# Kernel tuning notes

Measured on AMD Instinct MI355X. Metric: run time of the kernel, lower is better.

## Reference

```python
import jax, jax.numpy as jnp
import numpy as np

T, H_IN = 2048, 84
HID = 256
NA = 18


def _conv(x, w, b, stride):
    # x: [N,C,H,W], w: [O,I,kh,kw]
    y = jax.lax.conv_general_dilated(
        x, w, window_strides=(stride, stride), padding='VALID',
        dimension_numbers=('NCHW', 'OIHW', 'NCHW'))
    return jax.nn.relu(y + b[None, :, None, None])


def setup_inputs() -> dict:
    key = jax.random.key(0)
    ks = jax.random.split(key, 17)
    p = lambda k, shape, s=0.05: (jax.random.normal(k, shape, jnp.float32) * s)
    return {
        'input_frames': jax.random.uniform(ks[0], (T, 1, H_IN, H_IN), jnp.float32),
        'conv1_w': p(ks[1], (32, 1, 8, 8)),   'conv1_b': p(ks[2], (32,)),
        'conv2_w': p(ks[3], (64, 32, 4, 4)),  'conv2_b': p(ks[4], (64,)),
        'conv3_w': p(ks[5], (256, 64, 3, 3)), 'conv3_b': p(ks[6], (256,)),
        'attn_w1': p(ks[7], (HID, HID)),      'attn_b1': p(ks[8], (HID,)),
        'attn_w2': p(ks[9], (HID, HID)),      'attn_b2': p(ks[10], (HID,)),
        'lstm_w_ih': p(ks[11], (4 * HID, HID)), 'lstm_w_hh': p(ks[12], (4 * HID, HID)),
        'lstm_b_ih': p(ks[13], (4 * HID,)),     'lstm_b_hh': p(ks[14], (4 * HID,)),
        'q_w': p(ks[15], (NA, HID)),          'q_b': p(ks[16], (NA,)),
    }


def reference(input_frames, conv1_w, conv1_b, conv2_w, conv2_b, conv3_w, conv3_b,
              attn_w1, attn_b1, attn_w2, attn_b2,
              lstm_w_ih, lstm_w_hh, lstm_b_ih, lstm_b_hh, q_w, q_b):
    # CNN over all frames at once (loop in torch was over frames; math identical)
    x = _conv(input_frames, conv1_w, conv1_b, 4)   # [T,32,20,20]
    x = _conv(x, conv2_w, conv2_b, 2)              # [T,64,9,9]
    fm = _conv(x, conv3_w, conv3_b, 1)             # [T,256,7,7]
    t, c, hh, ww = fm.shape
    # build_vector: vectors[i, ch] = fm[ch, y, x], i = y*W + x
    vecs = fm.reshape(t, c, hh * ww).transpose(0, 2, 1)  # [T,49,256]

    def step(carry, v):
        h, cc = carry  # [256], [256]
        # additive attention; softmax over the 256 feature dim per spatial vector
        s = jnp.tanh(v @ attn_w1.T + attn_b1 + h)              # [49,256]
        w = jax.nn.softmax(s @ attn_w2.T + attn_b2, axis=-1)   # [49,256]
        ctx = jnp.sum(w * v, axis=0)                           # [256]
        # single-layer LSTM cell, torch gate order i,f,g,o
        gates = ctx @ lstm_w_ih.T + lstm_b_ih + h @ lstm_w_hh.T + lstm_b_hh
        i, f, g, o = jnp.split(gates, 4)
        c_new = jax.nn.sigmoid(f) * cc + jax.nn.sigmoid(i) * jnp.tanh(g)
        h_new = jax.nn.sigmoid(o) * jnp.tanh(c_new)
        return (h_new, c_new), None

    h0 = jnp.zeros((HID,), fm.dtype)
    (h_T, _), _ = jax.lax.scan(step, (h0, h0), vecs)
    q = h_T @ q_w.T + q_b          # [18]
    return q[None, :]              # [1, nr_actions], matches torch output
```

## Files before the change

kernel.cpp:

```cpp
#include <hip/hip_runtime.h>
#include <hip/hip_bf16.h>
#include <math.h>


#define T_FRAMES 2048
#define NI 49
#define HID 256
#define NA 18
#define NWG 8

typedef __bf16 v8bf __attribute__((ext_vector_type(8)));
typedef float v4f __attribute__((ext_vector_type(4)));

static constexpr size_t OFF_FM1   = 0;
static constexpr size_t OFF_FM2   = 104857600;
static constexpr size_t OFF_VECS  = 147324928;
static constexpr size_t OFF_W2B   = 250085376;
static constexpr size_t OFF_WIHB  = OFF_W2B  + 131072;
static constexpr size_t OFF_WHHB  = OFF_WIHB + 524288;
static constexpr size_t OFF_W1T   = OFF_WHHB + 524288;
static constexpr size_t OFF_HBUF  = OFF_FM2;
static constexpr size_t OFF_CPUB  = OFF_FM2 + 1024;
static constexpr size_t OFF_FLH   = OFF_FM2 + 9216;
static constexpr size_t OFF_FLC   = OFF_FM2 + 10240;

__global__ void prep_weights(const float* __restrict__ w2, const float* __restrict__ wih,
                             const float* __restrict__ whh, const float* __restrict__ w1,
                             __bf16* w2b, __bf16* wihb, __bf16* whhb, float* w1t) {
  int idx = blockIdx.x * 256 + threadIdx.x;
  int stride = gridDim.x * 256;
  for (int i = idx; i < 65536; i += stride) w2b[i] = (__bf16)w2[i];
  for (int i = idx; i < 262144; i += stride) wihb[i] = (__bf16)wih[i];
  for (int i = idx; i < 262144; i += stride) whhb[i] = (__bf16)whh[i];
  for (int i = idx; i < 65536; i += stride) {
    int r = i >> 8, c = i & 255;
    w1t[c * 256 + r] = w1[i];
  }
}

__global__ void conv1_k(const float* __restrict__ x, const float* __restrict__ w,
                        const float* __restrict__ b, float* __restrict__ y) {
  int idx = blockIdx.x * 256 + threadIdx.x;
  if (idx >= T_FRAMES * 32 * 20 * 20) return;
  int xx = idx % 20, yy = (idx / 20) % 20, o = (idx / 400) % 32, t = idx / 12800;
  const float* xp = x + t * 7056 + yy * 4 * 84 + xx * 4;
  const float* wp = w + o * 64;
  float acc = b[o];
  #pragma unroll
  for (int ky = 0; ky < 8; ky++)
    #pragma unroll
    for (int kx = 0; kx < 8; kx++)
      acc += xp[ky * 84 + kx] * wp[ky * 8 + kx];
  y[idx] = fmaxf(acc, 0.f);
}

__global__ __launch_bounds__(256) void conv2_k(const float* __restrict__ fm1, const float* __restrict__ w,
                                               const float* __restrict__ b, float* __restrict__ fm2) {
  __shared__ float xs[32 * 400];
  int t = blockIdx.x, tid = threadIdx.x;
  for (int i = tid; i < 12800; i += 256) xs[i] = fm1[t * 12800 + i];
  __syncthreads();
  int o = tid >> 2, q = tid & 3;
  int p0 = q * 21, p1 = (p0 + 21 < 81) ? p0 + 21 : 81;
  int ob[21];
  #pragma unroll
  for (int i2 = 0; i2 < 21; i2++) {
    int p = p0 + i2; if (p > 80) p = 80;
    int yy = p / 9, xx2 = p - yy * 9;
    ob[i2] = yy * 40 + xx2 * 2;
  }
  float acc[21];
  #pragma unroll
  for (int i2 = 0; i2 < 21; i2++) acc[i2] = 0.f;
  for (int c = 0; c < 32; c++) {
    int cbase = c * 400;
    for (int ky = 0; ky < 4; ky++)
      for (int kx = 0; kx < 4; kx++) {
        float wgt = w[((o * 32 + c) * 4 + ky) * 4 + kx];
        int kyo = ky * 20 + kx;
        #pragma unroll
        for (int i2 = 0; i2 < 21; i2++)
          acc[i2] += wgt * xs[cbase + ob[i2] + kyo];
      }
  }
  float bo = b[o];
  #pragma unroll
  for (int i2 = 0; i2 < 21; i2++) {
    int p = p0 + i2;
    if (p < p1) fm2[t * 5184 + o * 81 + p] = fmaxf(acc[i2] + bo, 0.f);
  }
}

__global__ __launch_bounds__(256) void conv3_k(const float* __restrict__ fm2, const float* __restrict__ w,
                                               const float* __restrict__ b, float* __restrict__ vecs) {
  __shared__ float xs[64 * 81];
  __shared__ float ws4[256][37];
  int t = blockIdx.x, tid = threadIdx.x;
  for (int i = tid; i < 64 * 81; i += 256) xs[i] = fm2[t * 5184 + i];
  float acc[49];
  #pragma unroll
  for (int i = 0; i < 49; i++) acc[i] = 0.f;
  for (int c0 = 0; c0 < 64; c0 += 4) {
    __syncthreads();
    for (int i = tid; i < 256 * 36; i += 256) {
      int oo = i / 36, j = i - oo * 36;
      ws4[oo][j] = w[oo * 576 + c0 * 9 + j];
    }
    __syncthreads();
    for (int cc = 0; cc < 4; cc++)
      for (int ky = 0; ky < 3; ky++)
        for (int kx = 0; kx < 3; kx++) {
          float wgt = ws4[tid][cc * 9 + ky * 3 + kx];
          const float* xp = &xs[(c0 + cc) * 81 + ky * 9 + kx];
          #pragma unroll
          for (int yy = 0; yy < 7; yy++)
            #pragma unroll
            for (int xx = 0; xx < 7; xx++)
              acc[yy * 7 + xx] += wgt * xp[yy * 9 + xx];
        }
  }
  float bo = b[tid];
  for (int i = 0; i < 49; i++)
    vecs[(t * 49 + i) * 256 + tid] = fmaxf(acc[i] + bo, 0.f);
}

__global__ __launch_bounds__(256) void aprep_k(const float* __restrict__ vecs, const float* __restrict__ w1t,
                                               const float* __restrict__ b1, float* __restrict__ A) {
  __shared__ float vs[49][256];
  int t = blockIdx.x, tid = threadIdx.x;
  for (int i = tid; i < 49 * 256; i += 256) vs[i >> 8][i & 255] = vecs[t * 12544 + i];
  __syncthreads();
  float acc[49];
  #pragma unroll
  for (int i = 0; i < 49; i++) acc[i] = 0.f;
  for (int k = 0; k < 256; k++) {
    float wgt = w1t[k * 256 + tid];
    #pragma unroll
    for (int i = 0; i < 49; i++) acc[i] += vs[i][k] * wgt;
  }
  float bb = b1[tid];
  for (int i = 0; i < 49; i++) A[(t * 49 + i) * 256 + tid] = acc[i] + bb;
}

__global__ void init_comm(unsigned* flh, unsigned* flc) {
  int idx = blockIdx.x * 512 + threadIdx.x;
  if (idx < NWG * 32) { flh[idx] = 0u; flc[idx] = 0u; }
}

__device__ __forceinline__ float tanh_fast(float x) {
  float e = __expf(2.f * x);
  return 1.f - 2.f / (e + 1.f);
}

__global__ __launch_bounds__(256, 1) void scan_k(
    const float* __restrict__ A, const float* __restrict__ vecs,
    const __bf16* __restrict__ w2b, const __bf16* __restrict__ wihb, const __bf16* __restrict__ whhb,
    const float* __restrict__ b2g, const float* __restrict__ bihg, const float* __restrict__ bhhg,
    const float* __restrict__ qw, const float* __restrict__ qb,
    float* hbuf, unsigned* cpub, unsigned* flh, unsigned* flc, float* out) {
  __shared__ __bf16 Ss[16][264];
  __shared__ float hs[HID];
  __shared__ __bf16 hbf[HID];
  __shared__ float Wt[8][HID];
  __shared__ float cxp[8][HID];
  __shared__ float b2s[HID];
  __shared__ float gb[4][32];

  const int w = blockIdx.x;
  const int tid = threadIdx.x;
  const int lane = tid & 63;
  const int wv = tid >> 6;
  const int quad = lane >> 4;
  const int l15 = lane & 15;
  const int r0 = 6 * w;
  const int nr = (w < 7) ? 6 : 7;
  const int prow = tid >> 5;
  const int pcol = (tid & 31) * 8;

  for (int i = tid; i < 16 * 264; i += 256) (&Ss[0][0])[i] = (__bf16)0.f;
  for (int i = tid; i < 8 * HID; i += 256) (&cxp[0][0])[i] = 0.f;
  b2s[tid] = b2g[tid];
  hs[tid] = 0.f;
  hbf[tid] = (__bf16)0.f;
  float cbias[4];
  if (tid < 32) {
    #pragma unroll
    for (int g = 0; g < 4; g++) {
      int row = 256 * g + 32 * w + tid;
      cbias[g] = bihg[row] + bhhg[row];
    }
  }
  float creg = 0.f;

  v8bf BW2[4][8];
  #pragma unroll
  for (int ntl = 0; ntl < 4; ntl++) {
    const int row = wv * 64 + ntl * 16 + l15;
    #pragma unroll
    for (int k = 0; k < 8; k++)
      BW2[ntl][k] = *(const v8bf*)(w2b + row * 256 + k * 32 + quad * 8);
  }
  v8bf BIH[2][8], BHH[2][8];
  #pragma unroll
  for (int nt = 0; nt < 2; nt++) {
    const int row = 256 * wv + 32 * w + nt * 16 + l15;
    #pragma unroll
    for (int k = 0; k < 8; k++) {
      BIH[nt][k] = *(const v8bf*)(wihb + row * 256 + k * 32 + quad * 8);
      BHH[nt][k] = *(const v8bf*)(whhb + row * 256 + k * 32 + quad * 8);
    }
  }
  __syncthreads();

  for (int t = 0; t < T_FRAMES; t++) {
    int rr = r0 + prow; if (rr > 48) rr = 48;
    const float* Ap = A + ((long)t * NI + rr) * HID + pcol;
    const float* Vp = vecs + ((long)t * NI + rr) * HID + pcol;
    const float4 a40 = *(const float4*)(Ap);
    const float4 a41 = *(const float4*)(Ap + 4);
    const float4 v40 = *(const float4*)(Vp);
    const float4 v41 = *(const float4*)(Vp + 4);

    if (t > 0) {
      if (wv == 0) {
        const unsigned tgt = (unsigned)t;
        int guard = 0;
        while (true) {
          unsigned fv = (lane < NWG)
              ? __hip_atomic_load(&flh[lane * 32], __ATOMIC_RELAXED, __HIP_MEMORY_SCOPE_AGENT)
              : tgt;
          if (__all(fv >= tgt) || ++guard > 5000000) break;
          __builtin_amdgcn_s_sleep(1);
        }
      }
      __syncthreads();
      float hv = __hip_atomic_load(&hbuf[tid], __ATOMIC_RELAXED, __HIP_MEMORY_SCOPE_AGENT);
      hs[tid] = hv;
      hbf[tid] = (__bf16)hv;
      __syncthreads();
    }

    if (prow < nr) {
      const float* hp = &hs[pcol];
      v8bf sv;
      sv[0] = (__bf16)tanh_fast(a40.x + hp[0]);
      sv[1] = (__bf16)tanh_fast(a40.y + hp[1]);
      sv[2] = (__bf16)tanh_fast(a40.z + hp[2]);
      sv[3] = (__bf16)tanh_fast(a40.w + hp[3]);
      sv[4] = (__bf16)tanh_fast(a41.x + hp[4]);
      sv[5] = (__bf16)tanh_fast(a41.y + hp[5]);
      sv[6] = (__bf16)tanh_fast(a41.z + hp[6]);
      sv[7] = (__bf16)tanh_fast(a41.w + hp[7]);
      *(v8bf*)&Ss[prow][pcol] = sv;
    }
    __syncthreads();

    v4f acc[4];
    #pragma unroll
    for (int ntl = 0; ntl < 4; ntl++) acc[ntl] = (v4f){0.f, 0.f, 0.f, 0.f};
    #pragma unroll
    for (int k = 0; k < 8; k++) {
      const v8bf av = *(const v8bf*)&Ss[l15][k * 32 + quad * 8];
      #pragma unroll
      for (int ntl = 0; ntl < 4; ntl++)
        acc[ntl] = __builtin_amdgcn_mfma_f32_16x16x32_bf16(av, BW2[ntl][k], acc[ntl], 0, 0, 0);
    }
    if (quad < 2) {
      #pragma unroll
      for (int ntl = 0; ntl < 4; ntl++) {
        const int col = wv * 64 + ntl * 16 + l15;
        const float bb = b2s[col];
        #pragma unroll
        for (int reg = 0; reg < 4; reg++)
          Wt[quad * 4 + reg][col] = acc[ntl][reg] + bb;
      }
    }
    __syncthreads();

    if (prow < nr) {
      float x[8];
      *(float4*)&x[0] = *(const float4*)&Wt[prow][pcol];
      *(float4*)&x[4] = *(const float4*)&Wt[prow][pcol + 4];
      float m = x[0];
      #pragma unroll
      for (int i = 1; i < 8; i++) m = fmaxf(m, x[i]);
      #pragma unroll
      for (int off = 16; off; off >>= 1) m = fmaxf(m, __shfl_xor(m, off, 64));
      float e[8], sm = 0.f;
      #pragma unroll
      for (int i = 0; i < 8; i++) { e[i] = __expf(x[i] - m); sm += e[i]; }
      #pragma unroll
      for (int off = 16; off; off >>= 1) sm += __shfl_xor(sm, off, 64);
      const float inv = 1.f / sm;
      cxp[prow][pcol + 0] = e[0] * inv * v40.x;
      cxp[prow][pcol + 1] = e[1] * inv * v40.y;
      cxp[prow][pcol + 2] = e[2] * inv * v40.z;
      cxp[prow][pcol + 3] = e[3] * inv * v40.w;
      cxp[prow][pcol + 4] = e[4] * inv * v41.x;
      cxp[prow][pcol + 5] = e[5] * inv * v41.y;
      cxp[prow][pcol + 6] = e[6] * inv * v41.z;
      cxp[prow][pcol + 7] = e[7] * inv * v41.w;
    }
    __syncthreads();

    float cp = 0.f;
    #pragma unroll
    for (int r = 0; r < 8; r++) cp += cxp[r][tid];
    float cpo = __shfl_xor(cp, 1, 64);
    if ((tid & 1) == 0) {
      union { __bf16 b; unsigned short s; } lo, hi;
      lo.b = (__bf16)cp; hi.b = (__bf16)cpo;
      unsigned u = ((unsigned)hi.s << 16) | (unsigned)lo.s;
      __hip_atomic_store(&cpub[w * 256 + (tid >> 1)], u, __ATOMIC_RELAXED, __HIP_MEMORY_SCOPE_AGENT);
    }
    __syncthreads();
    if (tid == 0)
      __hip_atomic_store(&flc[w * 32], (unsigned)(t + 1), __ATOMIC_RELEASE, __HIP_MEMORY_SCOPE_AGENT);

    v4f gacc[2];
    gacc[0] = (v4f){0.f, 0.f, 0.f, 0.f};
    gacc[1] = (v4f){0.f, 0.f, 0.f, 0.f};
    #pragma unroll
    for (int k = 0; k < 8; k++) {
      v8bf hf;
      #pragma unroll
      for (int z = 0; z < 8; z++) hf[z] = (__bf16)0.f;
      if (l15 == 0) hf = *(const v8bf*)&hbf[k * 32 + quad * 8];
      gacc[0] = __builtin_amdgcn_mfma_f32_16x16x32_bf16(hf, BHH[0][k], gacc[0], 0, 0, 0);
      gacc[1] = __builtin_amdgcn_mfma_f32_16x16x32_bf16(hf, BHH[1][k], gacc[1], 0, 0, 0);
    }

    {
      const unsigned tgt = (unsigned)(t + 1);
      int guard = 0;
      while (true) {
        unsigned fv = (lane < NWG)
            ? __hip_atomic_load(&flc[lane * 32], __ATOMIC_RELAXED, __HIP_MEMORY_SCOPE_AGENT)
            : tgt;
        if (__all(fv >= tgt) || ++guard > 5000000) break;
        __builtin_amdgcn_s_sleep(1);
      }
    }

    #pragma unroll
    for (int k = 0; k < 8; k++) {
      union { unsigned long long u[2]; v8bf v; } pf;
      pf.u[0] = 0ull; pf.u[1] = 0ull;
      if (l15 < NWG) {
        const unsigned long long* src =
            (const unsigned long long*)(cpub + l15 * 256) + (k * 8 + quad * 2);
        pf.u[0] = __hip_atomic_load(src, __ATOMIC_RELAXED, __HIP_MEMORY_SCOPE_AGENT);
        pf.u[1] = __hip_atomic_load(src + 1, __ATOMIC_RELAXED, __HIP_MEMORY_SCOPE_AGENT);
      }
      gacc[0] = __builtin_amdgcn_mfma_f32_16x16x32_bf16(pf.v, BIH[0][k], gacc[0], 0, 0, 0);
      gacc[1] = __builtin_amdgcn_mfma_f32_16x16x32_bf16(pf.v, BIH[1][k], gacc[1], 0, 0, 0);
    }
    #pragma unroll
    for (int nt = 0; nt < 2; nt++) {
      float tot = gacc[nt][0] + gacc[nt][1] + gacc[nt][2] + gacc[nt][3];
      tot += __shfl_xor(tot, 16, 64);
      tot += __shfl_xor(tot, 32, 64);
      if (lane < 16) gb[wv][nt * 16 + lane] = tot;
    }
    __syncthreads();

    if (tid < 32) {
      float gi = gb[0][tid] + cbias[0];
      float gf = gb[1][tid] + cbias[1];
      float gg = gb[2][tid] + cbias[2];
      float go = gb[3][tid] + cbias[3];
      float si = 1.f / (1.f + __expf(-gi));
      float sf = 1.f / (1.f + __expf(-gf));
      float so = 1.f / (1.f + __expf(-go));
      creg = sf * creg + si * tanh_fast(gg);
      float hn = so * tanh_fast(creg);
      __hip_atomic_store(&hbuf[32 * w + tid], hn, __ATOMIC_RELAXED, __HIP_MEMORY_SCOPE_AGENT);
    }
    __syncthreads();
    if (tid == 0)
      __hip_atomic_store(&flh[w * 32], (unsigned)(t + 1), __ATOMIC_RELEASE, __HIP_MEMORY_SCOPE_AGENT);
  }

  if (w == 0) {
    if (wv == 0) {
      const unsigned tgt = (unsigned)T_FRAMES;
      int guard = 0;
      while (true) {
        unsigned fv = (lane < NWG)
            ? __hip_atomic_load(&flh[lane * 32], __ATOMIC_RELAXED, __HIP_MEMORY_SCOPE_AGENT)
            : tgt;
        if (__all(fv >= tgt) || ++guard > 5000000) break;
        __builtin_amdgcn_s_sleep(1);
      }
    }
    __syncthreads();
    hs[tid] = __hip_atomic_load(&hbuf[tid], __ATOMIC_RELAXED, __HIP_MEMORY_SCOPE_AGENT);
    __syncthreads();
    if (tid < NA) {
      float acc = qb[tid];
      for (int k = 0; k < HID; k++) acc += hs[k] * qw[tid * HID + k];
      out[tid] = acc;
    }
  }
}

extern "C" void kernel_launch(void* const* d_in, const int* in_sizes, int n_in,
                              void* d_out, int out_size, void* d_ws, size_t ws_size,
                              hipStream_t stream) {
  const float* frames = (const float*)d_in[0];
  const float* c1w = (const float*)d_in[1];
  const float* c1b = (const float*)d_in[2];
  const float* c2w = (const float*)d_in[3];
  const float* c2b = (const float*)d_in[4];
  const float* c3w = (const float*)d_in[5];
  const float* c3b = (const float*)d_in[6];
  const float* aw1 = (const float*)d_in[7];
  const float* ab1 = (const float*)d_in[8];
  const float* aw2 = (const float*)d_in[9];
  const float* ab2 = (const float*)d_in[10];
  const float* wih = (const float*)d_in[11];
  const float* whh = (const float*)d_in[12];
  const float* bih = (const float*)d_in[13];
  const float* bhh = (const float*)d_in[14];
  const float* qw  = (const float*)d_in[15];
  const float* qb  = (const float*)d_in[16];

  char* ws = (char*)d_ws;
  float*  fm1   = (float*)(ws + OFF_FM1);
  float*  A     = (float*)(ws + OFF_FM1);
  float*  fm2   = (float*)(ws + OFF_FM2);
  float*  vecs  = (float*)(ws + OFF_VECS);
  __bf16* w2b   = (__bf16*)(ws + OFF_W2B);
  __bf16* wihb  = (__bf16*)(ws + OFF_WIHB);
  __bf16* whhb  = (__bf16*)(ws + OFF_WHHB);
  float*  w1t   = (float*)(ws + OFF_W1T);
  float*    hbuf = (float*)(ws + OFF_HBUF);
  unsigned* cpub = (unsigned*)(ws + OFF_CPUB);
  unsigned* flh  = (unsigned*)(ws + OFF_FLH);
  unsigned* flc  = (unsigned*)(ws + OFF_FLC);

  prep_weights<<<256, 256, 0, stream>>>(aw2, wih, whh, aw1, w2b, wihb, whhb, w1t);
  conv1_k<<<102400, 256, 0, stream>>>(frames, c1w, c1b, fm1);
  conv2_k<<<T_FRAMES, 256, 0, stream>>>(fm1, c2w, c2b, fm2);
  conv3_k<<<T_FRAMES, 256, 0, stream>>>(fm2, c3w, c3b, vecs);
  aprep_k<<<T_FRAMES, 256, 0, stream>>>(vecs, w1t, ab1, A);
  init_comm<<<1, 512, 0, stream>>>(flh, flc);
  scan_k<<<NWG, 256, 0, stream>>>(A, vecs, w2b, wihb, whhb, ab2, bih, bhh, qw, qb,
                                  hbuf, cpub, flh, flc, (float*)d_out);
}
```

Measured before the change: 16.41 ms.

## Replace flag-based inter-workgroup barriers with sequence-tagged 64-bit data words

Each value exchanged between the 8 scan workgroups is now packed with its step counter into one 64-bit atomic word. Consumers poll the data directly instead of waiting on separate release flags, which removes a flag store, a barrier and a round trip per step. Locally produced context values are read from shared memory rather than global. The grid becomes 57 blocks with only every eighth block active, apparently to place the workgroups on different XCDs or CUs. Divisions are replaced by the hardware reciprocal approximation, which costs some precision, and correctness now rests on 64-bit atomic stores being single-copy atomic.

```diff
diff --git a/kernel.cpp b/kernel.cpp
--- a/kernel.cpp
+++ b/kernel.cpp
@@ -20,9 +20,7 @@
 static constexpr size_t OFF_WHHB  = OFF_WIHB + 524288;
 static constexpr size_t OFF_W1T   = OFF_WHHB + 524288;
 static constexpr size_t OFF_HBUF  = OFF_FM2;
-static constexpr size_t OFF_CPUB  = OFF_FM2 + 1024;
-static constexpr size_t OFF_FLH   = OFF_FM2 + 9216;
-static constexpr size_t OFF_FLC   = OFF_FM2 + 10240;
+static constexpr size_t OFF_CPUB  = OFF_FM2 + 2048;
 
 __global__ void prep_weights(const float* __restrict__ w2, const float* __restrict__ wih,
                              const float* __restrict__ whh, const float* __restrict__ w1,
@@ -142,14 +140,18 @@
   for (int i = 0; i < 49; i++) A[(t * 49 + i) * 256 + tid] = acc[i] + bb;
 }
 
-__global__ void init_comm(unsigned* flh, unsigned* flc) {
-  int idx = blockIdx.x * 512 + threadIdx.x;
-  if (idx < NWG * 32) { flh[idx] = 0u; flc[idx] = 0u; }
+__global__ void init_comm(unsigned long long* hbuf, unsigned long long* cpub) {
+  int idx = blockIdx.x * 256 + threadIdx.x;
+  if (idx < 256) hbuf[idx] = 0ull;
+  if (idx < NWG * 128) cpub[idx] = 0ull;
 }
 
 __device__ __forceinline__ float tanh_fast(float x) {
   float e = __expf(2.f * x);
-  return 1.f - 2.f / (e + 1.f);
+  return 1.f - 2.f * __builtin_amdgcn_rcpf(e + 1.f);
+}
+__device__ __forceinline__ float sigm_fast(float x) {
+  return __builtin_amdgcn_rcpf(1.f + __expf(-x));
 }
 
 __global__ __launch_bounds__(256, 1) void scan_k(
@@ -157,7 +159,10 @@
     const __bf16* __restrict__ w2b, const __bf16* __restrict__ wihb, const __bf16* __restrict__ whhb,
     const float* __restrict__ b2g, const float* __restrict__ bihg, const float* __restrict__ bhhg,
     const float* __restrict__ qw, const float* __restrict__ qb,
-    float* hbuf, unsigned* cpub, unsigned* flh, unsigned* flc, float* out) {
+    unsigned long long* hbuf, unsigned long long* cpub, float* out) {
+  if (blockIdx.x & 7) return;
+  const int w = blockIdx.x >> 3;
+
   __shared__ __bf16 Ss[16][264];
   __shared__ float hs[HID];
   __shared__ __bf16 hbf[HID];
@@ -165,8 +170,8 @@
   __shared__ float cxp[8][HID];
   __shared__ float b2s[HID];
   __shared__ float gb[4][32];
-
-  const int w = blockIdx.x;
+  __shared__ unsigned cpl[128];
+
   const int tid = threadIdx.x;
   const int lane = tid & 63;
   const int wv = tid >> 6;
@@ -222,19 +227,15 @@
     const float4 v41 = *(const float4*)(Vp + 4);
 
     if (t > 0) {
-      if (wv == 0) {
-        const unsigned tgt = (unsigned)t;
-        int guard = 0;
-        while (true) {
-          unsigned fv = (lane < NWG)
-              ? __hip_atomic_load(&flh[lane * 32], __ATOMIC_RELAXED, __HIP_MEMORY_SCOPE_AGENT)
-              : tgt;
-          if (__all(fv >= tgt) || ++guard > 5000000) break;
-          __builtin_amdgcn_s_sleep(1);
-        }
-      }
-      __syncthreads();
-      float hv = __hip_atomic_load(&hbuf[tid], __ATOMIC_RELAXED, __HIP_MEMORY_SCOPE_AGENT);
+      const unsigned tgt = (unsigned)t;
+      unsigned long long pk =
+          __hip_atomic_load(&hbuf[tid], __ATOMIC_RELAXED, __HIP_MEMORY_SCOPE_AGENT);
+      int guard = 0;
+      while ((unsigned)(pk >> 32) < tgt && ++guard < 5000000) {
+        __builtin_amdgcn_s_sleep(1);
+        pk = __hip_atomic_load(&hbuf[tid], __ATOMIC_RELAXED, __HIP_MEMORY_SCOPE_AGENT);
+      }
+      float hv = __uint_as_float((unsigned)pk);
       hs[tid] = hv;
       hbf[tid] = (__bf16)hv;
       __syncthreads();
@@ -291,7 +292,7 @@
       for (int i = 0; i < 8; i++) { e[i] = __expf(x[i] - m); sm += e[i]; }
       #pragma unroll
       for (int off = 16; off; off >>= 1) sm += __shfl_xor(sm, off, 64);
-      const float inv = 1.f / sm;
+      const float inv = __builtin_amdgcn_rcpf(sm);
       cxp[prow][pcol + 0] = e[0] * inv * v40.x;
       cxp[prow][pcol + 1] = e[1] * inv * v40.y;
       cxp[prow][pcol + 2] = e[2] * inv * v40.z;
@@ -307,15 +308,29 @@
     #pragma unroll
     for (int r = 0; r < 8; r++) cp += cxp[r][tid];
     float cpo = __shfl_xor(cp, 1, 64);
+    unsigned word = 0u;
     if ((tid & 1) == 0) {
       union { __bf16 b; unsigned short s; } lo, hi;
       lo.b = (__bf16)cp; hi.b = (__bf16)cpo;
-      unsigned u = ((unsigned)hi.s << 16) | (unsigned)lo.s;
-      __hip_atomic_store(&cpub[w * 256 + (tid >> 1)], u, __ATOMIC_RELAXED, __HIP_MEMORY_SCOPE_AGENT);
-    }
-    __syncthreads();
-    if (tid == 0)
-      __hip_atomic_store(&flc[w * 32], (unsigned)(t + 1), __ATOMIC_RELEASE, __HIP_MEMORY_SCOPE_AGENT);
+      word = ((unsigned)hi.s << 16) | (unsigned)lo.s;
+      unsigned long long pk =
+          ((unsigned long long)(unsigned)(t + 1) << 32) | (unsigned long long)word;
+      __hip_atomic_store(&cpub[w * 128 + (tid >> 1)], pk, __ATOMIC_RELAXED, __HIP_MEMORY_SCOPE_AGENT);
+      cpl[tid >> 1] = word;
+    }
+    __syncthreads();
+
+    unsigned long long g[8][4];
+    const unsigned ctgt = (unsigned)(t + 1);
+    const bool remote = (l15 < NWG) && (l15 != w);
+    if (remote) {
+      const unsigned long long* src = cpub + l15 * 128 + quad * 4;
+      #pragma unroll
+      for (int k = 0; k < 8; k++)
+        #pragma unroll
+        for (int q2 = 0; q2 < 4; q2++)
+          g[k][q2] = __hip_atomic_load(&src[k * 16 + q2], __ATOMIC_RELAXED, __HIP_MEMORY_SCOPE_AGENT);
+    }
 
     v4f gacc[2];
     gacc[0] = (v4f){0.f, 0.f, 0.f, 0.f};
@@ -331,26 +346,47 @@
     }
 
     {
-      const unsigned tgt = (unsigned)(t + 1);
-      int guard = 0;
-      while (true) {
-        unsigned fv = (lane < NWG)
-            ? __hip_atomic_load(&flc[lane * 32], __ATOMIC_RELAXED, __HIP_MEMORY_SCOPE_AGENT)
-            : tgt;
-        if (__all(fv >= tgt) || ++guard > 5000000) break;
-        __builtin_amdgcn_s_sleep(1);
+      bool ok = true;
+      if (remote) {
+        #pragma unroll
+        for (int k = 0; k < 8; k++)
+          #pragma unroll
+          for (int q2 = 0; q2 < 4; q2++)
+            ok &= ((unsigned)(g[k][q2] >> 32) >= ctgt);
+      }
+      if (!__all(ok)) {
+        int guard = 0;
+        while (true) {
+          __builtin_amdgcn_s_sleep(1);
+          ok = true;
+          if (remote) {
+            const unsigned long long* src = cpub + l15 * 128 + quad * 4;
+            #pragma unroll
+            for (int k = 0; k < 8; k++)
+              #pragma unroll
+              for (int q2 = 0; q2 < 4; q2++) {
+                g[k][q2] = __hip_atomic_load(&src[k * 16 + q2], __ATOMIC_RELAXED, __HIP_MEMORY_SCOPE_AGENT);
+                ok &= ((unsigned)(g[k][q2] >> 32) >= ctgt);
+              }
+          }
+          if (__all(ok) || ++guard > 5000000) break;
+        }
       }
     }
 
     #pragma unroll
     for (int k = 0; k < 8; k++) {
-      union { unsigned long long u[2]; v8bf v; } pf;
-      pf.u[0] = 0ull; pf.u[1] = 0ull;
-      if (l15 < NWG) {
-        const unsigned long long* src =
-            (const unsigned long long*)(cpub + l15 * 256) + (k * 8 + quad * 2);
-        pf.u[0] = __hip_atomic_load(src, __ATOMIC_RELAXED, __HIP_MEMORY_SCOPE_AGENT);
-        pf.u[1] = __hip_atomic_load(src + 1, __ATOMIC_RELAXED, __HIP_MEMORY_SCOPE_AGENT);
+      union { unsigned u[4]; v8bf v; } pf;
+      if (remote) {
+        pf.u[0] = (unsigned)g[k][0]; pf.u[1] = (unsigned)g[k][1];
+        pf.u[2] = (unsigned)g[k][2]; pf.u[3] = (unsigned)g[k][3];
+      } else if (l15 == w) {
+        pf.u[0] = cpl[k * 16 + quad * 4 + 0];
+        pf.u[1] = cpl[k * 16 + quad * 4 + 1];
+        pf.u[2] = cpl[k * 16 + quad * 4 + 2];
+        pf.u[3] = cpl[k * 16 + quad * 4 + 3];
+      } else {
+        pf.u[0] = pf.u[1] = pf.u[2] = pf.u[3] = 0u;
       }
       gacc[0] = __builtin_amdgcn_mfma_f32_16x16x32_bf16(pf.v, BIH[0][k], gacc[0], 0, 0, 0);
       gacc[1] = __builtin_amdgcn_mfma_f32_16x16x32_bf16(pf.v, BIH[1][k], gacc[1], 0, 0, 0);
@@ -369,32 +405,27 @@
       float gf = gb[1][tid] + cbias[1];
       float gg = gb[2][tid] + cbias[2];
       float go = gb[3][tid] + cbias[3];
-      float si = 1.f / (1.f + __expf(-gi));
-      float sf = 1.f / (1.f + __expf(-gf));
-      float so = 1.f / (1.f + __expf(-go));
+      float si = sigm_fast(gi);
+      float sf = sigm_fast(gf);
+      float so = sigm_fast(go);
       creg = sf * creg + si * tanh_fast(gg);
       float hn = so * tanh_fast(creg);
-      __hip_atomic_store(&hbuf[32 * w + tid], hn, __ATOMIC_RELAXED, __HIP_MEMORY_SCOPE_AGENT);
-    }
-    __syncthreads();
-    if (tid == 0)
-      __hip_atomic_store(&flh[w * 32], (unsigned)(t + 1), __ATOMIC_RELEASE, __HIP_MEMORY_SCOPE_AGENT);
+      unsigned long long pk = ((unsigned long long)(unsigned)(t + 1) << 32) |
+                              (unsigned long long)__float_as_uint(hn);
+      __hip_atomic_store(&hbuf[32 * w + tid], pk, __ATOMIC_RELAXED, __HIP_MEMORY_SCOPE_AGENT);
+    }
   }
 
   if (w == 0) {
-    if (wv == 0) {
-      const unsigned tgt = (unsigned)T_FRAMES;
-      int guard = 0;
-      while (true) {
-        unsigned fv = (lane < NWG)
-            ? __hip_atomic_load(&flh[lane * 32], __ATOMIC_RELAXED, __HIP_MEMORY_SCOPE_AGENT)
-            : tgt;
-        if (__all(fv >= tgt) || ++guard > 5000000) break;
-        __builtin_amdgcn_s_sleep(1);
-      }
-    }
-    __syncthreads();
-    hs[tid] = __hip_atomic_load(&hbuf[tid], __ATOMIC_RELAXED, __HIP_MEMORY_SCOPE_AGENT);
+    const unsigned tgt = (unsigned)T_FRAMES;
+    unsigned long long pk =
+        __hip_atomic_load(&hbuf[tid], __ATOMIC_RELAXED, __HIP_MEMORY_SCOPE_AGENT);
+    int guard = 0;
+    while ((unsigned)(pk >> 32) < tgt && ++guard < 5000000) {
+      __builtin_amdgcn_s_sleep(1);
+      pk = __hip_atomic_load(&hbuf[tid], __ATOMIC_RELAXED, __HIP_MEMORY_SCOPE_AGENT);
+    }
+    hs[tid] = __uint_as_float((unsigned)pk);
     __syncthreads();
     if (tid < NA) {
       float acc = qb[tid];
@@ -434,17 +465,15 @@
   __bf16* wihb  = (__bf16*)(ws + OFF_WIHB);
   __bf16* whhb  = (__bf16*)(ws + OFF_WHHB);
   float*  w1t   = (float*)(ws + OFF_W1T);
-  float*    hbuf = (float*)(ws + OFF_HBUF);
-  unsigned* cpub = (unsigned*)(ws + OFF_CPUB);
-  unsigned* flh  = (unsigned*)(ws + OFF_FLH);
-  unsigned* flc  = (unsigned*)(ws + OFF_FLC);
+  unsigned long long* hbuf = (unsigned long long*)(ws + OFF_HBUF);
+  unsigned long long* cpub = (unsigned long long*)(ws + OFF_CPUB);
 
   prep_weights<<<256, 256, 0, stream>>>(aw2, wih, whh, aw1, w2b, wihb, whhb, w1t);
   conv1_k<<<102400, 256, 0, stream>>>(frames, c1w, c1b, fm1);
   conv2_k<<<T_FRAMES, 256, 0, stream>>>(fm1, c2w, c2b, fm2);
   conv3_k<<<T_FRAMES, 256, 0, stream>>>(fm2, c3w, c3b, vecs);
   aprep_k<<<T_FRAMES, 256, 0, stream>>>(vecs, w1t, ab1, A);
-  init_comm<<<1, 512, 0, stream>>>(flh, flc);
-  scan_k<<<NWG, 256, 0, stream>>>(A, vecs, w2b, wihb, whhb, ab2, bih, bhh, qw, qb,
-                                  hbuf, cpub, flh, flc, (float*)d_out);
-}
+  init_comm<<<4, 256, 0, stream>>>(hbuf, cpub);
+  scan_k<<<57, 256, 0, stream>>>(A, vecs, w2b, wihb, whhb, ab2, bih, bhh, qw, qb,
+                                 hbuf, cpub, (float*)d_out);
+}
```

Measured after the change: 17.37 ms. 5.9% more time.
